# Performance work log

Measured on AMD Instinct MI355X. Metric: run time of the kernel, lower is better.

Reference implementation:

```python
import jax, jax.numpy as jnp
import numpy as np

# RasterConfig constants (from init_kwargs)
H, W = 128, 128
G = 2048
ALPHA_THR = 1.0 / 255.0          # meta_f32[0]
T_THR = 1e-4                     # meta_f32[1] transmittance_threshold
ALPHA_MAX = 0.99                 # meta_f32[6] alpha clamp
BG = jnp.array([0.0, 0.0, 0.0], dtype=jnp.float32)  # meta_f32[2:5]


def setup_inputs() -> dict:
    key = jax.random.key(0)
    k = jax.random.split(key, 7)
    # gaussian centers spread over the image (in pixel coords)
    means2d = jax.random.uniform(k[0], (G, 2), dtype=jnp.float32) * jnp.array([W, H], dtype=jnp.float32)
    # build positive-definite conics = inverse of random 2D covariances
    sx = jax.random.uniform(k[1], (G,), minval=1.0, maxval=8.0, dtype=jnp.float32)
    sy = jax.random.uniform(k[2], (G,), minval=1.0, maxval=8.0, dtype=jnp.float32)
    rho = jax.random.uniform(k[3], (G,), minval=-0.7, maxval=0.7, dtype=jnp.float32)
    sxx, syy, sxy = sx * sx, sy * sy, rho * sx * sy
    det = sxx * syy - sxy * sxy
    conics = jnp.stack([syy / det, -sxy / det, sxx / det], axis=1).astype(jnp.float32)  # (a,b,c)
    colors = jax.random.uniform(k[4], (G, 3), dtype=jnp.float32)
    opacities = jax.random.uniform(k[5], (G,), minval=0.05, maxval=0.95, dtype=jnp.float32)
    depths = jax.random.uniform(k[6], (G,), minval=0.1, maxval=10.0, dtype=jnp.float32)
    return {"means2d": means2d, "conics": conics, "colors": colors,
            "opacities": opacities, "depths": depths}


def reference(means2d, conics, colors, opacities, depths):
    # depth sort, front-to-back (torch.argsort ascending, stable)
    order = jnp.argsort(depths, stable=True)
    m = means2d[order]            # [G,2]
    con = conics[order]           # [G,3] -> (a,b,c)
    col = colors[order]           # [G,3]
    op = opacities[order]         # [G]

    # pixel centers
    xs = jnp.arange(W, dtype=jnp.float32) + 0.5
    ys = jnp.arange(H, dtype=jnp.float32) + 0.5
    gy, gx = jnp.meshgrid(ys, xs, indexing='ij')
    px = gx.reshape(-1)           # [P], P = H*W
    py = gy.reshape(-1)

    dx = px[:, None] - m[None, :, 0]   # [P,G]
    dy = py[:, None] - m[None, :, 1]
    a, b, c = con[:, 0], con[:, 1], con[:, 2]
    # 0.5 * d^T Sigma^{-1} d with conic (a,b,c)
    sigma = 0.5 * (a * dx * dx + c * dy * dy) + b * dx * dy
    alpha = jnp.minimum(op * jnp.exp(-sigma), ALPHA_MAX)
    # skip invalid quadratic form and sub-threshold alphas
    alpha = jnp.where((sigma < 0.0) | (alpha < ALPHA_THR), 0.0, alpha)

    one_m = 1.0 - alpha
    cp = jnp.cumprod(one_m, axis=1)
    T_before = jnp.concatenate(
        [jnp.ones((px.shape[0], 1), jnp.float32), cp[:, :-1]], axis=1)  # exclusive cumprod
    # early-termination: a gaussian whose inclusion would push T below threshold
    # (and all subsequent ones) is skipped. Terminated set is a suffix since T is
    # monotone nonincreasing, so T_before is exact on the surviving prefix.
    valid = (T_before * one_m) >= T_THR
    w = jnp.where(valid, alpha, 0.0) * T_before     # [P,G] compositing weights
    rgb = w @ col                                    # [P,3]
    final_T = jnp.prod(jnp.where(valid, one_m, 1.0), axis=1)
    img = rgb + final_T[:, None] * BG
    return img.reshape(H, W, 3)
```

## Files before the change

kernel.cpp:

```cpp
#include <hip/hip_runtime.h>
#include <hip/hip_bf16.h>
#include <hip/hip_fp16.h>

#define G_COUNT 2048
#define IMG_W 128
#define T_THR 1e-4f
#define ALPHA_MAX 0.99f
#define LOG2E 1.4426950408889634f
#define INV255 0.003921568627451f

__device__ __forceinline__ float fexp2(float x) {
#if __has_builtin(__builtin_amdgcn_exp2f)
    return __builtin_amdgcn_exp2f(x);
#else
    return __expf(x * 0.6931471805599453f);
#endif
}

__device__ __forceinline__ float frcp(float x) {
#if __has_builtin(__builtin_amdgcn_rcpf)
    return __builtin_amdgcn_rcpf(x);
#else
    return 1.0f / x;
#endif
}

__device__ __forceinline__ float clampf(float x, float lo, float hi) {
    return fminf(fmaxf(x, lo), hi);
}

__global__ __launch_bounds__(512)
void raster_fused(const float* __restrict__ means2d,
                  const float* __restrict__ conics,
                  const float* __restrict__ colors,
                  const float* __restrict__ opac,
                  const float* __restrict__ depths,
                  float* __restrict__ out) {
    __shared__ alignas(16) float4 s_rec[2 * (G_COUNT + 1)];
    __shared__ alignas(16) unsigned long long s_key[G_COUNT + 2];
    __shared__ alignas(16) int s_perm[G_COUNT];
    __shared__ float s_T[2][8][64];
    __shared__ float s_rgb[8][192];
    __shared__ int s_cnt;

    const int tid = threadIdx.x;
    const int wv = tid >> 6;
    const int lane = tid & 63;
    const int tile = blockIdx.x;
    const int tx = tile & 15;
    const int ty = tile >> 4;

    if (tid == 0) s_cnt = 0;
    __syncthreads();

    const float bx0 = (float)(tx * 8) + 0.5f;
    const float bx1 = (float)(tx * 8 + 7) + 0.5f;
    const float by0 = (float)(ty * 8) + 0.5f;
    const float by1 = (float)(ty * 8 + 7) + 0.5f;

    for (int k = 0; k < G_COUNT; k += 512) {
        int gi = k + tid;
        float2 m = ((const float2*)means2d)[gi];
        float a = conics[3 * gi + 0];
        float b = conics[3 * gi + 1];
        float c = conics[3 * gi + 2];
        float o = opac[gi];
        float d = depths[gi];

        float A = 0.5f * a * LOG2E;
        float C = 0.5f * c * LOG2E;
        float B = b * LOG2E;
        float l2o = __log2f(255.0f * o);

        float lx = bx0 - m.x, hx = bx1 - m.x;
        float ly = by0 - m.y, hy = by1 - m.y;
        bool inside = (lx <= 0.0f) & (hx >= 0.0f) & (ly <= 0.0f) & (hy >= 0.0f);
        float rC = frcp(C), rA = frcp(A);
        float d1 = clampf(-0.5f * B * lx * rC, ly, hy);
        float d2 = clampf(-0.5f * B * hx * rC, ly, hy);
        float d3 = clampf(-0.5f * B * ly * rA, lx, hx);
        float d4 = clampf(-0.5f * B * hy * rA, lx, hx);
        float m1 = fmaf(A * lx, lx, fmaf(C * d1, d1, (B * lx) * d1));
        float m2 = fmaf(A * hx, hx, fmaf(C * d2, d2, (B * hx) * d2));
        float m3 = fmaf(A * d3, d3, fmaf(C * ly, ly, (B * d3) * ly));
        float m4 = fmaf(A * d4, d4, fmaf(C * hy, hy, (B * d4) * hy));
        float minv = fminf(fminf(m1, m2), fminf(m3, m4));
        bool pass = inside || (minv <= l2o + 0.01f);

        unsigned long long msk = __ballot(pass);
        int prefix = __builtin_amdgcn_mbcnt_hi((unsigned)(msk >> 32),
                     __builtin_amdgcn_mbcnt_lo((unsigned)msk, 0));
        int wbase = 0;
        if (lane == 0) wbase = atomicAdd(&s_cnt, __popcll(msk));
        wbase = __shfl(wbase, 0);
        if (pass) {
            int pos = wbase + prefix;
            __half2 rg = __floats2half2_rn(colors[3 * gi + 0], colors[3 * gi + 1]);
            __half2 bz = __floats2half2_rn(colors[3 * gi + 2], 0.0f);
            s_rec[2 * pos + 0] = make_float4(m.x, m.y, A, C);
            s_rec[2 * pos + 1] = make_float4(B, l2o,
                                             __uint_as_float(*(unsigned*)&rg),
                                             __uint_as_float(*(unsigned*)&bz));
            s_key[pos] = ((unsigned long long)__float_as_uint(d) << 32) | (unsigned)gi;
        }
    }
    __syncthreads();

    const int n = s_cnt;
    const int npad = (n + 63) & ~63;
    if (tid < 2) s_key[n + tid] = ~0ULL;
    __syncthreads();
    const int npairs = (n + 1) >> 1;
    for (int s = tid; s < n; s += 512) {
        unsigned long long key = s_key[s];
        int rk = 0;
        const ulonglong2* kp = (const ulonglong2*)s_key;
#pragma unroll 4
        for (int jj = 0; jj < npairs; ++jj) {
            ulonglong2 k2 = kp[jj];
            rk += (k2.x < key) ? 1 : 0;
            rk += (k2.y < key) ? 1 : 0;
        }
        s_perm[rk] = s;
    }
    for (int i = n + tid; i < npad; i += 512) s_perm[i] = n;
    if (tid == 0 && n < G_COUNT) {
        s_rec[2 * n + 0] = make_float4(0.f, 0.f, 0.f, 0.f);
        s_rec[2 * n + 1] = make_float4(0.f, -1.f, 0.f, 0.f);
    }
    __syncthreads();

    const int pxi = tx * 8 + (lane & 7);
    const int pyi = ty * 8 + (lane >> 3);
    const float px = (float)pxi + 0.5f;
    const float py = (float)pyi + 0.5f;

    float T = 1.0f;
    float accr = 0.0f, accg = 0.0f, accb = 0.0f;
    const int ngroups = npad >> 6;

    for (int g = 0; g < ngroups; ++g) {
        const int base = g * 64 + wv * 8;
        const int4* pp4 = (const int4*)(s_perm + base);
        int4 pa = pp4[0], pb = pp4[1];
        int pidx[8] = {pa.x, pa.y, pa.z, pa.w, pb.x, pb.y, pb.z, pb.w};

        float4 ra[8], rb[8];
#pragma unroll
        for (int j = 0; j < 8; ++j) {
            ra[j] = s_rec[2 * pidx[j] + 0];
            rb[j] = s_rec[2 * pidx[j] + 1];
        }
        float al[8], cum[8];
        float run = 1.0f;
#pragma unroll
        for (int j = 0; j < 8; ++j) {
            float dx = px - ra[j].x;
            float dy = py - ra[j].y;
            float s2 = fmaf(ra[j].z * dx, dx, fmaf(ra[j].w * dy, dy, (rb[j].x * dx) * dy));
            float a = fminf(fexp2(rb[j].y - s2) * INV255, ALPHA_MAX);
            a = (s2 < 0.0f || s2 > rb[j].y) ? 0.0f : a;
            al[j] = a;
            run *= 1.0f - a;
            cum[j] = run;
        }
        s_T[g & 1][wv][lane] = run;
        __syncthreads();

        float pre = 1.0f, full = 1.0f;
#pragma unroll
        for (int t = 0; t < 8; ++t) {
            float v = s_T[g & 1][t][lane];
            full *= v;
            if (t < wv) pre *= v;
        }
        float Tw0 = T * pre;
#pragma unroll
        for (int j = 0; j < 8; ++j) {
            float Tb = Tw0 * ((j == 0) ? 1.0f : cum[j - 1]);
            float Tn = Tw0 * cum[j];
            float w = (Tn >= T_THR) ? al[j] * Tb : 0.0f;
            unsigned urg = __float_as_uint(rb[j].z);
            unsigned ub = __float_as_uint(rb[j].w);
            float2 rg = __half22float2(*(__half2*)&urg);
            float2 b2 = __half22float2(*(__half2*)&ub);
            accr = fmaf(w, rg.x, accr);
            accg = fmaf(w, rg.y, accg);
            accb = fmaf(w, b2.x, accb);
        }
        T *= full;
        if (__ballot(T >= T_THR) == 0ULL) break;
    }

    s_rgb[wv][lane * 3 + 0] = accr;
    s_rgb[wv][lane * 3 + 1] = accg;
    s_rgb[wv][lane * 3 + 2] = accb;
    __syncthreads();

    if (tid < 192) {
        float sum = 0.0f;
#pragma unroll
        for (int w = 0; w < 8; ++w) sum += s_rgb[w][tid];
        int p2 = tid / 3;
        int ch = tid - p2 * 3;
        int opx = tx * 8 + (p2 & 7);
        int opy = ty * 8 + (p2 >> 3);
        out[((size_t)opy * IMG_W + opx) * 3 + ch] = sum;
    }
}

extern "C" void kernel_launch(void* const* d_in, const int* in_sizes, int n_in,
                              void* d_out, int out_size, void* d_ws, size_t ws_size,
                              hipStream_t stream) {
    const float* means2d = (const float*)d_in[0];
    const float* conics  = (const float*)d_in[1];
    const float* colors  = (const float*)d_in[2];
    const float* opac    = (const float*)d_in[3];
    const float* depths  = (const float*)d_in[4];
    float* out = (float*)d_out;

    raster_fused<<<256, 512, 0, stream>>>(means2d, conics, colors, opac, depths, out);
}
```

Baseline: 14.15 us.

## Split rank sort across thread pairs with 32-bit keys and prefetch next group

The rank-counting sort now uses 32-bit depth keys, with a separate index array instead of packed 64-bit keys. Each key is ranked by two threads that each scan half the list, and their counts are combined with a shuffle. Ties are detected by an equality count and resolved by a rare linear rescan on gaussian index. The compositing loop is double-buffered so the next group's permutation and records are loaded from shared memory before the barrier, overlapping LDS latency with the barrier and the accumulation work. This costs extra registers for two record sets, which may lower occupancy, and adds 8 KB of shared memory for the index array.

```diff
diff --git a/kernel.cpp b/kernel.cpp
--- a/kernel.cpp
+++ b/kernel.cpp
@@ -37,7 +37,8 @@
                   const float* __restrict__ depths,
                   float* __restrict__ out) {
     __shared__ alignas(16) float4 s_rec[2 * (G_COUNT + 1)];
-    __shared__ alignas(16) unsigned long long s_key[G_COUNT + 2];
+    __shared__ alignas(16) unsigned s_key[G_COUNT + 4];
+    __shared__ alignas(16) unsigned s_idx[G_COUNT];
     __shared__ alignas(16) int s_perm[G_COUNT];
     __shared__ float s_T[2][8][64];
     __shared__ float s_rgb[8][192];
@@ -101,27 +102,48 @@
             s_rec[2 * pos + 1] = make_float4(B, l2o,
                                              __uint_as_float(*(unsigned*)&rg),
                                              __uint_as_float(*(unsigned*)&bz));
-            s_key[pos] = ((unsigned long long)__float_as_uint(d) << 32) | (unsigned)gi;
+            s_key[pos] = __float_as_uint(d);
+            s_idx[pos] = (unsigned)gi;
         }
     }
     __syncthreads();
 
     const int n = s_cnt;
     const int npad = (n + 63) & ~63;
-    if (tid < 2) s_key[n + tid] = ~0ULL;
-    __syncthreads();
-    const int npairs = (n + 1) >> 1;
-    for (int s = tid; s < n; s += 512) {
-        unsigned long long key = s_key[s];
-        int rk = 0;
-        const ulonglong2* kp = (const ulonglong2*)s_key;
+    if (tid < 4) s_key[n + tid] = 0xFFFFFFFFu;
+    __syncthreads();
+    {
+        const int nq = (n + 3) >> 2;
+        const int half = tid & 1;
+        const int qlo = half ? (nq >> 1) : 0;
+        const int qhi = half ? nq : (nq >> 1);
+        const uint4* kq = (const uint4*)s_key;
+        for (int s0 = tid >> 1; s0 < n; s0 += 256) {
+            unsigned key = s_key[s0];
+            int rk = 0, eq = 0;
 #pragma unroll 4
-        for (int jj = 0; jj < npairs; ++jj) {
-            ulonglong2 k2 = kp[jj];
-            rk += (k2.x < key) ? 1 : 0;
-            rk += (k2.y < key) ? 1 : 0;
+            for (int q = qlo; q < qhi; ++q) {
+                uint4 k4 = kq[q];
+                rk += (k4.x < key) ? 1 : 0;
+                rk += (k4.y < key) ? 1 : 0;
+                rk += (k4.z < key) ? 1 : 0;
+                rk += (k4.w < key) ? 1 : 0;
+                eq += (k4.x == key) ? 1 : 0;
+                eq += (k4.y == key) ? 1 : 0;
+                eq += (k4.z == key) ? 1 : 0;
+                eq += (k4.w == key) ? 1 : 0;
+            }
+            rk += __shfl_xor(rk, 1);
+            eq += __shfl_xor(eq, 1);
+            if (half == 0) {
+                if (eq > 1) {
+                    unsigned mygi = s_idx[s0];
+                    for (int j = 0; j < n; ++j)
+                        rk += (s_key[j] == key && s_idx[j] < mygi) ? 1 : 0;
+                }
+                s_perm[rk] = s0;
+            }
         }
-        s_perm[rk] = s;
     }
     for (int i = n + tid; i < npad; i += 512) s_perm[i] = n;
     if (tid == 0 && n < G_COUNT) {
@@ -139,57 +161,75 @@
     float accr = 0.0f, accg = 0.0f, accb = 0.0f;
     const int ngroups = npad >> 6;
 
-    for (int g = 0; g < ngroups; ++g) {
-        const int base = g * 64 + wv * 8;
-        const int4* pp4 = (const int4*)(s_perm + base);
-        int4 pa = pp4[0], pb = pp4[1];
-        int pidx[8] = {pa.x, pa.y, pa.z, pa.w, pb.x, pb.y, pb.z, pb.w};
-
-        float4 ra[8], rb[8];
-#pragma unroll
-        for (int j = 0; j < 8; ++j) {
-            ra[j] = s_rec[2 * pidx[j] + 0];
-            rb[j] = s_rec[2 * pidx[j] + 1];
+#define LOAD_GRP(P, RA, RB, gbase)                                          \
+    {                                                                       \
+        const int4* _pp4 = (const int4*)(s_perm + (gbase));                 \
+        int4 _pa = _pp4[0], _pb = _pp4[1];                                  \
+        P[0] = _pa.x; P[1] = _pa.y; P[2] = _pa.z; P[3] = _pa.w;             \
+        P[4] = _pb.x; P[5] = _pb.y; P[6] = _pb.z; P[7] = _pb.w;             \
+        _Pragma("unroll")                                                   \
+        for (int _j = 0; _j < 8; ++_j) {                                    \
+            RA[_j] = s_rec[2 * P[_j] + 0];                                  \
+            RB[_j] = s_rec[2 * P[_j] + 1];                                  \
+        }                                                                   \
+    }
+
+#define PROC_GRP(RA, RB, NP, NRA, NRB, g)                                   \
+    {                                                                       \
+        float al[8], cum[8];                                                \
+        float run = 1.0f;                                                   \
+        _Pragma("unroll")                                                   \
+        for (int j = 0; j < 8; ++j) {                                       \
+            float dx = px - RA[j].x;                                        \
+            float dy = py - RA[j].y;                                        \
+            float s2 = fmaf(RA[j].z * dx, dx,                               \
+                            fmaf(RA[j].w * dy, dy, (RB[j].x * dx) * dy));   \
+            float a = fminf(fexp2(RB[j].y - s2) * INV255, ALPHA_MAX);       \
+            a = (s2 < 0.0f || s2 > RB[j].y) ? 0.0f : a;                     \
+            al[j] = a;                                                      \
+            run *= 1.0f - a;                                                \
+            cum[j] = run;                                                   \
+        }                                                                   \
+        s_T[(g) & 1][wv][lane] = run;                                       \
+        int _gn = ((g) + 1 < ngroups) ? (g) + 1 : (g);                      \
+        LOAD_GRP(NP, NRA, NRB, _gn * 64 + wv * 8)             \
+        __syncthreads();                                                    \
+        float pre = 1.0f, full = 1.0f;                                      \
+        _Pragma("unroll")                                                   \
+        for (int t = 0; t < 8; ++t) {                                       \
+            float v = s_T[(g) & 1][t][lane];                                \
+            full *= v;                       \
+            if (t < wv) pre *= v;                                           \
+        }                                                                   \
+        float Tw0 = T * pre;                       \
+        _Pragma("unroll")                                                   \
+        for (int j = 0; j < 8; ++j) {                                       \
+            float Tb = Tw0 * ((j == 0) ? 1.0f : cum[j - 1]);                \
+            float Tn = Tw0 * cum[j];                                        \
+            float w = (Tn >= T_THR) ? al[j] * Tb : 0.0f;                    \
+            unsigned urg = __float_as_uint(RB[j].z);                        \
+            unsigned ub = __float_as_uint(RB[j].w);                         \
+            float2 rg = __half22float2(*(__half2*)&urg);                    \
+            float2 b2 = __half22float2(*(__half2*)&ub);                     \
+            accr = fmaf(w, rg.x, accr);                                     \
+            accg = fmaf(w, rg.y, accg);                                     \
+            accb = fmaf(w, b2.x, accb);                                     \
+        }                                                                   \
+        T *= full;                            \
+        if (__ballot(T >= T_THR) == 0ULL) break;      \
+    }
+
+    {
+        int pA[8], pB[8];
+        float4 raA[8], rbA[8], raB[8], rbB[8];
+        if (ngroups > 0) LOAD_GRP(pA, raA, rbA, wv * 8)
+        for (int g = 0; g < ngroups; ++g) {
+            if (g & 1) {
+                PROC_GRP(raB, rbB, pA, raA, rbA, g)
+            } else {
+                PROC_GRP(raA, rbA, pB, raB, rbB, g)
+            }
         }
-        float al[8], cum[8];
-        float run = 1.0f;
-#pragma unroll
-        for (int j = 0; j < 8; ++j) {
-            float dx = px - ra[j].x;
-            float dy = py - ra[j].y;
-            float s2 = fmaf(ra[j].z * dx, dx, fmaf(ra[j].w * dy, dy, (rb[j].x * dx) * dy));
-            float a = fminf(fexp2(rb[j].y - s2) * INV255, ALPHA_MAX);
-            a = (s2 < 0.0f || s2 > rb[j].y) ? 0.0f : a;
-            al[j] = a;
-            run *= 1.0f - a;
-            cum[j] = run;
-        }
-        s_T[g & 1][wv][lane] = run;
-        __syncthreads();
-
-        float pre = 1.0f, full = 1.0f;
-#pragma unroll
-        for (int t = 0; t < 8; ++t) {
-            float v = s_T[g & 1][t][lane];
-            full *= v;
-            if (t < wv) pre *= v;
-        }
-        float Tw0 = T * pre;
-#pragma unroll
-        for (int j = 0; j < 8; ++j) {
-            float Tb = Tw0 * ((j == 0) ? 1.0f : cum[j - 1]);
-            float Tn = Tw0 * cum[j];
-            float w = (Tn >= T_THR) ? al[j] * Tb : 0.0f;
-            unsigned urg = __float_as_uint(rb[j].z);
-            unsigned ub = __float_as_uint(rb[j].w);
-            float2 rg = __half22float2(*(__half2*)&urg);
-            float2 b2 = __half22float2(*(__half2*)&ub);
-            accr = fmaf(w, rg.x, accr);
-            accg = fmaf(w, rg.y, accg);
-            accb = fmaf(w, b2.x, accb);
-        }
-        T *= full;
-        if (__ballot(T >= T_THR) == 0ULL) break;
     }
 
     s_rgb[wv][lane * 3 + 0] = accr;
```

New measurement: 14.24 us. Within noise of the previous version (+0.7%).
